# Performance work log

Measured on AMD Instinct MI355X. Metric: run time of the kernel, lower is better.

The kernel has to match this reference:

```python
import jax, jax.numpy as jnp
import numpy as np


def setup_inputs() -> dict:
    key = jax.random.key(0)
    k1, k2, k3, k4 = jax.random.split(key, 4)
    B, N, Fin, Fout, K = 8, 256, 64, 64, 3
    H = jax.random.normal(k1, (B, N, N, Fin), dtype=jnp.float32)
    # static Chebyshev polynomial stacks T_0..T_{K-1} for origin / dest Laplacians
    cheb_L1 = jax.random.normal(k2, (K, N, N), dtype=jnp.float32) * 0.1
    cheb_L2 = jax.random.normal(k3, (K, N, N), dtype=jnp.float32) * 0.1
    # xavier_uniform over last two dims (fan_in=Fin, fan_out=Fout)
    limit = float(np.sqrt(6.0 / (Fin + Fout)))
    weights = jax.random.uniform(k4, (K, K, Fin, Fout), dtype=jnp.float32,
                                 minval=-limit, maxval=limit)
    bias = jnp.zeros((Fout,), dtype=jnp.float32)
    return {"H": H, "cheb_L1": cheb_L1, "cheb_L2": cheb_L2,
            "weights": weights, "bias": bias}


def reference(H, cheb_L1, cheb_L2, weights, bias):
    # H' = relu( sum_{i,j} T_i(L1) @_1 H @_2 T_j(L2) @_3 W_ij + b )
    # Step 1: left graph shift for all i at once: (K,B,N,N,F)
    H_x1 = jnp.einsum('kuv,bvwf->kbuwf', cheb_L1, H)
    # Step 2+3 fused: right shift by T_j, project by W_ij, accumulate over i,j
    out = jnp.einsum('kbuwf,lwz,klfo->buzo', H_x1, cheb_L2, weights)
    return jax.nn.relu(out + bias)
```

## Files before the change

kernel.cpp:

```cpp
#include <hip/hip_runtime.h>

typedef __attribute__((ext_vector_type(8))) short s16x8;
typedef __attribute__((ext_vector_type(4))) float f32x4;

#define MFMA16 __builtin_amdgcn_mfma_f32_16x16x32_bf16

__device__ __forceinline__ short f2bf(float x) {
  union { float f; unsigned u; } c; c.f = x;
  unsigned r = (c.u + 0x7fffu + ((c.u >> 16) & 1u)) >> 16;
  return (short)r;
}

__device__ __forceinline__ void gld16(const void* g, void* l) {
  __builtin_amdgcn_global_load_lds(
      (const __attribute__((address_space(1))) unsigned*)g,
      (__attribute__((address_space(3))) unsigned*)l, 16, 0, 0);
}


__global__ __launch_bounds__(256) void k_cvt_l1(const float* __restrict__ L1,
                                                short* __restrict__ L1b) {
  int i = blockIdx.x * 256 + threadIdx.x;
  L1b[i] = f2bf(L1[i]);
}

__global__ __launch_bounds__(256) void k_build_l2cat(const float* __restrict__ L2,
                                                     short* __restrict__ L2cat) {
  __shared__ float t[32][33];
  const int l = blockIdx.z, w0 = blockIdx.x * 32, z0 = blockIdx.y * 32;
  const int tx = threadIdx.x, ty = threadIdx.y;
  const float* src = L2 + (size_t)l * 65536;
  for (int i = ty; i < 32; i += 8) t[i][tx] = src[(size_t)(w0 + i) * 256 + z0 + tx];
  __syncthreads();
  for (int i = ty; i < 32; i += 8)
    L2cat[(size_t)(z0 + i) * 768 + l * 256 + w0 + tx] = f2bf(t[tx][i]);
}

__global__ __launch_bounds__(256) void k_build_wt(const float* __restrict__ W,
                                                  short* __restrict__ WT) {
  for (int idx = threadIdx.x + blockIdx.x * 256; idx < 192 * 192; idx += 256 * gridDim.x) {
    int lo = idx / 192, kf = idx % 192;
    int l = lo >> 6, o = lo & 63, k = kf / 64, f = kf & 63;
    WT[idx] = f2bf(W[(((size_t)(k * 3 + l) * 64 + f) << 6) + o]);
  }
}

__global__ __launch_bounds__(256) void k_cvt_ht(const float* __restrict__ H,
                                                short* __restrict__ HbT, int b0) {
  __shared__ float t[32][33];
  const int bc = blockIdx.z;
  const int wf0 = blockIdx.x * 32, v0 = blockIdx.y * 32;
  const int tx = threadIdx.x, ty = threadIdx.y;
  const float* src = H + ((size_t)(b0 + bc) * 256 + v0) * 16384;
  for (int i = ty; i < 32; i += 8) t[i][tx] = src[(size_t)i * 16384 + wf0 + tx];
  __syncthreads();
  short* dst = HbT + ((size_t)bc * 16384 + wf0) * 256;
  for (int i = ty; i < 32; i += 8) dst[(size_t)i * 256 + v0 + tx] = f2bf(t[tx][i]);
}

__global__ __launch_bounds__(256) void k_s1(const short* __restrict__ L1b,
                                            const short* __restrict__ HbT,
                                            short* __restrict__ A2) {
  __shared__ __align__(16) short At[128 * 32];
  __shared__ __align__(16) short Bt[128 * 32];
  const int t = threadIdx.x, lane = t & 63, wid = t >> 6;
  const int n0 = blockIdx.x * 128;
  const int kk = blockIdx.y >> 1;
  const int u0 = (blockIdx.y & 1) * 128;
  const int bc = blockIdx.z;
  const short* Ag = L1b + (size_t)kk * 65536;
  const short* Bg = HbT + (size_t)bc * 16384 * 256;
  const int wm = wid >> 1, wn = wid & 1;
  const int srow = lane >> 2;
  const int selem = ((lane & 3) ^ ((lane >> 3) & 3)) * 8;
  const int koff = (((lane >> 4) ^ ((lane >> 1) & 3)) * 8);
  f32x4 acc[4][4] = {};
  for (int kt = 0; kt < 256; kt += 32) {
#pragma unroll
    for (int j = 0; j < 2; ++j) {
      const int rb = wid * 32 + j * 16;
      gld16(Ag + (size_t)(u0 + rb + srow) * 256 + kt + selem, (short*)At + (size_t)rb * 32);
      gld16(Bg + (size_t)(n0 + rb + srow) * 256 + kt + selem, (short*)Bt + (size_t)rb * 32);
    }
    __syncthreads();
    const int ar = lane & 15;
    s16x8 a[4], b[4];
#pragma unroll
    for (int i = 0; i < 4; ++i) a[i] = *(const s16x8*)&At[(wm * 64 + i * 16 + ar) * 32 + koff];
#pragma unroll
    for (int j = 0; j < 4; ++j) b[j] = *(const s16x8*)&Bt[(wn * 64 + j * 16 + ar) * 32 + koff];
#pragma unroll
    for (int i = 0; i < 4; ++i)
#pragma unroll
      for (int j = 0; j < 4; ++j) acc[i][j] = MFMA16(a[i], b[j], acc[i][j], 0, 0, 0);
    __syncthreads();
  }
  const int cr = lane >> 4, cc = lane & 15;
#pragma unroll
  for (int i = 0; i < 4; ++i)
#pragma unroll
    for (int j = 0; j < 4; ++j) {
      const int ncol = n0 + wn * 64 + j * 16 + cc;
      const int w = ncol >> 6, f = ncol & 63;
#pragma unroll
      for (int r = 0; r < 4; ++r) {
        const int u = u0 + wm * 64 + i * 16 + cr * 4 + r;
        A2[(((size_t)bc * 256 + u) * 256 + w) * 192 + kk * 64 + f] = f2bf(acc[i][j][r]);
      }
    }
}

__global__ __launch_bounds__(512) void k_s23(const short* __restrict__ A2,
                                             const short* __restrict__ WT,
                                             const short* __restrict__ L2cat,
                                             const float* __restrict__ bias,
                                             float* __restrict__ out, int b0) {
  __shared__ __align__(16) short P[64 * 768];
  __shared__ __align__(16) short At[256 * 64];
  __shared__ __align__(16) short Bs[192 * 64];
  const int t = threadIdx.x, lane = t & 63, wid = t >> 6;
  const int bul = blockIdx.x;
  const int ar = lane & 15, cc = lane & 15, cr = lane >> 4;
  const int selem = ((lane & 7) ^ ((lane >> 3) & 7)) * 8;
  const int ko0 = (((lane >> 4)) ^ (lane & 7)) * 8;
  const int ko1 = ((4 + (lane >> 4)) ^ (lane & 7)) * 8;
  const int srow8 = lane >> 3;

  f32x4 acc[3][2][4] = {};
  const short* A2g = A2 + (size_t)bul * 256 * 192;
  for (int kt = 0; kt < 192; kt += 64) {
#pragma unroll
    for (int is = 0; is < 4; ++is) {
      const int rb = wid * 32 + is * 8;
      gld16(A2g + (size_t)(rb + srow8) * 192 + kt + selem, (short*)At + (size_t)rb * 64);
    }
#pragma unroll
    for (int is = 0; is < 3; ++is) {
      const int rb = wid * 24 + is * 8;
      gld16(WT + (size_t)(rb + srow8) * 192 + kt + selem, (short*)Bs + (size_t)rb * 64);
    }
    __syncthreads();
    s16x8 a0[2], a1[2];
#pragma unroll
    for (int i = 0; i < 2; ++i) {
      a0[i] = *(const s16x8*)&At[(wid * 32 + i * 16 + ar) * 64 + ko0];
      a1[i] = *(const s16x8*)&At[(wid * 32 + i * 16 + ar) * 64 + ko1];
    }
#pragma unroll
    for (int l = 0; l < 3; ++l)
#pragma unroll
      for (int j = 0; j < 4; ++j) {
        s16x8 b0v = *(const s16x8*)&Bs[(l * 64 + j * 16 + ar) * 64 + ko0];
        s16x8 b1v = *(const s16x8*)&Bs[(l * 64 + j * 16 + ar) * 64 + ko1];
#pragma unroll
        for (int i = 0; i < 2; ++i) {
          acc[l][i][j] = MFMA16(a0[i], b0v, acc[l][i][j], 0, 0, 0);
          acc[l][i][j] = MFMA16(a1[i], b1v, acc[l][i][j], 0, 0, 0);
        }
      }
    __syncthreads();
  }
#pragma unroll
  for (int l = 0; l < 3; ++l)
#pragma unroll
    for (int i = 0; i < 2; ++i)
#pragma unroll
      for (int j = 0; j < 4; ++j)
#pragma unroll
        for (int rp = 0; rp < 2; ++rp) {
          const int r = rp * 2;
          const int w = wid * 32 + i * 16 + cr * 4 + r;
          const int o = j * 16 + cc;
          const int lw = l * 256 + w;
          const int addr = o * 768 + ((lw >> 3) ^ (o & 7)) * 8 + (lw & 7);
          unsigned lo16 = (unsigned short)f2bf(acc[l][i][j][r]);
          unsigned hi16 = (unsigned short)f2bf(acc[l][i][j][r + 1]);
          *(unsigned*)&P[addr] = lo16 | (hi16 << 16);
        }
  __syncthreads();

  f32x4 acc2[2][4] = {};
  for (int kt = 0; kt < 768; kt += 64) {
#pragma unroll
    for (int is = 0; is < 4; ++is) {
      const int rb = wid * 32 + is * 8;
      gld16(L2cat + (size_t)(rb + srow8) * 768 + kt + selem, (short*)At + (size_t)rb * 64);
    }
    __syncthreads();
    s16x8 a0[2], a1[2];
#pragma unroll
    for (int i = 0; i < 2; ++i) {
      a0[i] = *(const s16x8*)&At[(wid * 32 + i * 16 + ar) * 64 + ko0];
      a1[i] = *(const s16x8*)&At[(wid * 32 + i * 16 + ar) * 64 + ko1];
    }
#pragma unroll
    for (int j = 0; j < 4; ++j) {
      s16x8 b0v = *(const s16x8*)&P[(j * 16 + ar) * 768 + kt + ko0];
      s16x8 b1v = *(const s16x8*)&P[(j * 16 + ar) * 768 + kt + ko1];
#pragma unroll
      for (int i = 0; i < 2; ++i) {
        acc2[i][j] = MFMA16(a0[i], b0v, acc2[i][j], 0, 0, 0);
        acc2[i][j] = MFMA16(a1[i], b1v, acc2[i][j], 0, 0, 0);
      }
    }
    __syncthreads();
  }
  const int bu_g = b0 * 256 + bul;
  float* og = out + (size_t)bu_g * 256 * 64;
#pragma unroll
  for (int i = 0; i < 2; ++i)
#pragma unroll
    for (int j = 0; j < 4; ++j) {
      const float bv = bias[j * 16 + cc];
#pragma unroll
      for (int r = 0; r < 4; ++r) {
        const int z = wid * 32 + i * 16 + cr * 4 + r;
        og[(size_t)z * 64 + j * 16 + cc] = fmaxf(acc2[i][j][r] + bv, 0.f);
      }
    }
}

extern "C" void kernel_launch(void* const* d_in, const int* in_sizes, int n_in,
                              void* d_out, int out_size, void* d_ws, size_t ws_size,
                              hipStream_t stream) {
  const float* H    = (const float*)d_in[0];
  const float* L1   = (const float*)d_in[1];
  const float* L2   = (const float*)d_in[2];
  const float* W    = (const float*)d_in[3];
  const float* bias = (const float*)d_in[4];
  float* out = (float*)d_out;

  char* ws = (char*)d_ws;
  short* L1b   = (short*)ws;
  short* L2cat = (short*)(ws + (384 << 10));
  short* WT    = (short*)(ws + (768 << 10));
  char* data = ws + (4ull << 20);

  const size_t perb = 32ull << 20;
  size_t avail = (ws_size > (4ull << 20)) ? ws_size - (4ull << 20) : 0;
  int nb = 1;
  if (avail >= 8 * perb) nb = 8;
  else if (avail >= 4 * perb) nb = 4;
  else if (avail >= 2 * perb) nb = 2;

  short* HbT = (short*)data;
  short* A2  = (short*)(data + (size_t)nb * (8ull << 20));

  k_cvt_l1<<<768, 256, 0, stream>>>(L1, L1b);
  k_build_l2cat<<<dim3(8, 8, 3), dim3(32, 8), 0, stream>>>(L2, L2cat);
  k_build_wt<<<36, 256, 0, stream>>>(W, WT);

  for (int b0 = 0; b0 < 8; b0 += nb) {
    k_cvt_ht<<<dim3(512, 8, nb), dim3(32, 8), 0, stream>>>(H, HbT, b0);
    k_s1<<<dim3(128, 6, nb), 256, 0, stream>>>(L1b, HbT, A2);
    k_s23<<<nb * 256, 512, 0, stream>>>(A2, WT, L2cat, bias, out, b0);
  }
}
```

Before: 334.3 us.

## Double-buffer LDS loads in both GEMM kernels and split output channels across blocks

k_s1 gets double-buffered LDS tiles so the next K-slice global-to-LDS load overlaps the current MFMAs, with one barrier fewer per step. k_s23 is restructured: the grid doubles so each block handles half of the 64 output channels, and the full weight slice is preloaded into LDS. A2 and L2cat tiles are double-buffered with explicit vmcnt waits, and LDS is aliased to cut footprint so more blocks can be resident. The cost is redundant A2 and L2cat reads per half, and the intra-loop sync relies on vmcnt without workgroup barriers, which risks a race between waves sharing buffers.

```diff
diff --git a/kernel.cpp b/kernel.cpp
--- a/kernel.cpp
+++ b/kernel.cpp
@@ -4,6 +4,7 @@
 typedef __attribute__((ext_vector_type(4))) float f32x4;
 
 #define MFMA16 __builtin_amdgcn_mfma_f32_16x16x32_bf16
+#define WAIT_VM0() asm volatile("s_waitcnt vmcnt(0)" ::: "memory")
 
 __device__ __forceinline__ short f2bf(float x) {
   union { float f; unsigned u; } c; c.f = x;
@@ -58,11 +59,11 @@
   for (int i = ty; i < 32; i += 8) dst[(size_t)i * 256 + v0 + tx] = f2bf(t[tx][i]);
 }
 
-__global__ __launch_bounds__(256) void k_s1(const short* __restrict__ L1b,
-                                            const short* __restrict__ HbT,
-                                            short* __restrict__ A2) {
-  __shared__ __align__(16) short At[128 * 32];
-  __shared__ __align__(16) short Bt[128 * 32];
+__global__ __launch_bounds__(256, 4) void k_s1(const short* __restrict__ L1b,
+                                               const short* __restrict__ HbT,
+                                               short* __restrict__ A2) {
+  __shared__ __align__(16) short At[2][128 * 32];
+  __shared__ __align__(16) short Bt[2][128 * 32];
   const int t = threadIdx.x, lane = t & 63, wid = t >> 6;
   const int n0 = blockIdx.x * 128;
   const int kk = blockIdx.y >> 1;
@@ -73,22 +74,34 @@
   const int wm = wid >> 1, wn = wid & 1;
   const int srow = lane >> 2;
   const int selem = ((lane & 3) ^ ((lane >> 3) & 3)) * 8;
-  const int koff = (((lane >> 4) ^ ((lane >> 1) & 3)) * 8);
+  const int koff = ((lane >> 4) ^ ((lane >> 1) & 3)) * 8;
+  const int ar = lane & 15;
+#pragma unroll
+  for (int j = 0; j < 2; ++j) {
+    const int rb = wid * 32 + j * 16;
+    gld16(Ag + (size_t)(u0 + rb + srow) * 256 + selem, At[0] + rb * 32);
+    gld16(Bg + (size_t)(n0 + rb + srow) * 256 + selem, Bt[0] + rb * 32);
+  }
+  __syncthreads();
   f32x4 acc[4][4] = {};
-  for (int kt = 0; kt < 256; kt += 32) {
-#pragma unroll
-    for (int j = 0; j < 2; ++j) {
-      const int rb = wid * 32 + j * 16;
-      gld16(Ag + (size_t)(u0 + rb + srow) * 256 + kt + selem, (short*)At + (size_t)rb * 32);
-      gld16(Bg + (size_t)(n0 + rb + srow) * 256 + kt + selem, (short*)Bt + (size_t)rb * 32);
-    }
-    __syncthreads();
-    const int ar = lane & 15;
+#pragma unroll
+  for (int kt8 = 0; kt8 < 8; ++kt8) {
+    const int cur = kt8 & 1;
     s16x8 a[4], b[4];
 #pragma unroll
-    for (int i = 0; i < 4; ++i) a[i] = *(const s16x8*)&At[(wm * 64 + i * 16 + ar) * 32 + koff];
-#pragma unroll
-    for (int j = 0; j < 4; ++j) b[j] = *(const s16x8*)&Bt[(wn * 64 + j * 16 + ar) * 32 + koff];
+    for (int i = 0; i < 4; ++i)
+      a[i] = *(const s16x8*)&At[cur][(wm * 64 + i * 16 + ar) * 32 + koff];
+#pragma unroll
+    for (int j = 0; j < 4; ++j)
+      b[j] = *(const s16x8*)&Bt[cur][(wn * 64 + j * 16 + ar) * 32 + koff];
+    if (kt8 < 7) {
+#pragma unroll
+      for (int j = 0; j < 2; ++j) {
+        const int rb = wid * 32 + j * 16;
+        gld16(Ag + (size_t)(u0 + rb + srow) * 256 + (kt8 + 1) * 32 + selem, At[cur ^ 1] + rb * 32);
+        gld16(Bg + (size_t)(n0 + rb + srow) * 256 + (kt8 + 1) * 32 + selem, Bt[cur ^ 1] + rb * 32);
+      }
+    }
 #pragma unroll
     for (int i = 0; i < 4; ++i)
 #pragma unroll
@@ -110,62 +123,74 @@
     }
 }
 
-__global__ __launch_bounds__(512) void k_s23(const short* __restrict__ A2,
-                                             const short* __restrict__ WT,
-                                             const short* __restrict__ L2cat,
-                                             const float* __restrict__ bias,
-                                             float* __restrict__ out, int b0) {
-  __shared__ __align__(16) short P[64 * 768];
-  __shared__ __align__(16) short At[256 * 64];
-  __shared__ __align__(16) short Bs[192 * 64];
+__global__ __launch_bounds__(512, 4) void k_s23(const short* __restrict__ A2,
+                                                const short* __restrict__ WTg,
+                                                const short* __restrict__ L2cat,
+                                                const float* __restrict__ bias,
+                                                float* __restrict__ out, int b0) {
+  __shared__ __align__(16) char lds[81920];
+  short* P   = (short*)lds;
+  short* Ws  = (short*)lds;
+  short* AtS = (short*)(lds + 49152);
   const int t = threadIdx.x, lane = t & 63, wid = t >> 6;
-  const int bul = blockIdx.x;
-  const int ar = lane & 15, cc = lane & 15, cr = lane >> 4;
-  const int selem = ((lane & 7) ^ ((lane >> 3) & 7)) * 8;
-  const int ko0 = (((lane >> 4)) ^ (lane & 7)) * 8;
-  const int ko1 = ((4 + (lane >> 4)) ^ (lane & 7)) * 8;
-  const int srow8 = lane >> 3;
-
-  f32x4 acc[3][2][4] = {};
-  const short* A2g = A2 + (size_t)bul * 256 * 192;
-  for (int kt = 0; kt < 192; kt += 64) {
-#pragma unroll
-    for (int is = 0; is < 4; ++is) {
-      const int rb = wid * 32 + is * 8;
-      gld16(A2g + (size_t)(rb + srow8) * 192 + kt + selem, (short*)At + (size_t)rb * 64);
-    }
-#pragma unroll
-    for (int is = 0; is < 3; ++is) {
-      const int rb = wid * 24 + is * 8;
-      gld16(WT + (size_t)(rb + srow8) * 192 + kt + selem, (short*)Bs + (size_t)rb * 64);
-    }
-    __syncthreads();
-    s16x8 a0[2], a1[2];
-#pragma unroll
-    for (int i = 0; i < 2; ++i) {
-      a0[i] = *(const s16x8*)&At[(wid * 32 + i * 16 + ar) * 64 + ko0];
-      a1[i] = *(const s16x8*)&At[(wid * 32 + i * 16 + ar) * 64 + ko1];
-    }
+  const int bx = blockIdx.x;
+  const int bul = (bx & 7) | ((bx >> 4) << 3);
+  const int o0 = ((bx >> 3) & 1) * 32;
+  const int ar = lane & 15, cc = ar, cr = lane >> 4, sl = lane & 7;
+  const int srow = lane >> 2;
+  const int selem = ((lane & 3) ^ ((lane >> 3) & 3)) * 8;
+  const int koff = ((lane >> 4) ^ ((lane >> 1) & 3)) * 8;
+  const short* A2g = A2 + (size_t)bul * 49152;
+
+  for (int s = wid; s < 36; s += 8) {
+    const int t6 = s / 6, rb = (s % 6) * 16;
+    const int gr = (rb >> 5) * 64 + o0 + (rb & 31);
+    gld16(WTg + (size_t)(gr + srow) * 192 + t6 * 32 + selem, Ws + (t6 * 96 + rb) * 32);
+  }
+#pragma unroll
+  for (int is = 0; is < 2; ++is)
+    gld16(A2g + (size_t)(wid * 32 + is * 16 + srow) * 192 + selem,
+          AtS + (wid * 32 + is * 16) * 32);
+  __syncthreads();
+
+  f32x4 acc[3][2][2] = {};
+#pragma unroll
+  for (int kt6 = 0; kt6 < 6; ++kt6) {
+    const int cur = kt6 & 1;
+    WAIT_VM0();
+    s16x8 a[2];
+#pragma unroll
+    for (int i = 0; i < 2; ++i)
+      a[i] = *(const s16x8*)&AtS[(cur * 256 + wid * 32 + i * 16 + ar) * 32 + koff];
+    s16x8 b[3][2];
 #pragma unroll
     for (int l = 0; l < 3; ++l)
 #pragma unroll
-      for (int j = 0; j < 4; ++j) {
-        s16x8 b0v = *(const s16x8*)&Bs[(l * 64 + j * 16 + ar) * 64 + ko0];
-        s16x8 b1v = *(const s16x8*)&Bs[(l * 64 + j * 16 + ar) * 64 + ko1];
-#pragma unroll
-        for (int i = 0; i < 2; ++i) {
-          acc[l][i][j] = MFMA16(a0[i], b0v, acc[l][i][j], 0, 0, 0);
-          acc[l][i][j] = MFMA16(a1[i], b1v, acc[l][i][j], 0, 0, 0);
-        }
-      }
-    __syncthreads();
-  }
+      for (int j = 0; j < 2; ++j)
+        b[l][j] = *(const s16x8*)&Ws[(kt6 * 96 + l * 32 + j * 16 + ar) * 32 + koff];
+    if (kt6 < 5) {
+#pragma unroll
+      for (int is = 0; is < 2; ++is)
+        gld16(A2g + (size_t)(wid * 32 + is * 16 + srow) * 192 + (kt6 + 1) * 32 + selem,
+              AtS + ((cur ^ 1) * 256 + wid * 32 + is * 16) * 32);
+    }
+#pragma unroll
+    for (int l = 0; l < 3; ++l)
+#pragma unroll
+      for (int j = 0; j < 2; ++j)
+#pragma unroll
+        for (int i = 0; i < 2; ++i)
+          acc[l][j][i] = MFMA16(a[i], b[l][j], acc[l][j][i], 0, 0, 0);
+  }
+
+  __syncthreads();
+
 #pragma unroll
   for (int l = 0; l < 3; ++l)
 #pragma unroll
-    for (int i = 0; i < 2; ++i)
-#pragma unroll
-      for (int j = 0; j < 4; ++j)
+    for (int j = 0; j < 2; ++j)
+#pragma unroll
+      for (int i = 0; i < 2; ++i)
 #pragma unroll
         for (int rp = 0; rp < 2; ++rp) {
           const int r = rp * 2;
@@ -173,49 +198,53 @@
           const int o = j * 16 + cc;
           const int lw = l * 256 + w;
           const int addr = o * 768 + ((lw >> 3) ^ (o & 7)) * 8 + (lw & 7);
-          unsigned lo16 = (unsigned short)f2bf(acc[l][i][j][r]);
-          unsigned hi16 = (unsigned short)f2bf(acc[l][i][j][r + 1]);
+          unsigned lo16 = (unsigned short)f2bf(acc[l][j][i][r]);
+          unsigned hi16 = (unsigned short)f2bf(acc[l][j][i][r + 1]);
           *(unsigned*)&P[addr] = lo16 | (hi16 << 16);
         }
-  __syncthreads();
-
-  f32x4 acc2[2][4] = {};
-  for (int kt = 0; kt < 768; kt += 64) {
-#pragma unroll
-    for (int is = 0; is < 4; ++is) {
-      const int rb = wid * 32 + is * 8;
-      gld16(L2cat + (size_t)(rb + srow8) * 768 + kt + selem, (short*)At + (size_t)rb * 64);
-    }
-    __syncthreads();
-    s16x8 a0[2], a1[2];
-#pragma unroll
-    for (int i = 0; i < 2; ++i) {
-      a0[i] = *(const s16x8*)&At[(wid * 32 + i * 16 + ar) * 64 + ko0];
-      a1[i] = *(const s16x8*)&At[(wid * 32 + i * 16 + ar) * 64 + ko1];
-    }
-#pragma unroll
-    for (int j = 0; j < 4; ++j) {
-      s16x8 b0v = *(const s16x8*)&P[(j * 16 + ar) * 768 + kt + ko0];
-      s16x8 b1v = *(const s16x8*)&P[(j * 16 + ar) * 768 + kt + ko1];
-#pragma unroll
-      for (int i = 0; i < 2; ++i) {
-        acc2[i][j] = MFMA16(a0[i], b0v, acc2[i][j], 0, 0, 0);
-        acc2[i][j] = MFMA16(a1[i], b1v, acc2[i][j], 0, 0, 0);
-      }
-    }
-    __syncthreads();
-  }
-  const int bu_g = b0 * 256 + bul;
-  float* og = out + (size_t)bu_g * 256 * 64;
+#pragma unroll
+  for (int is = 0; is < 2; ++is)
+    gld16(L2cat + (size_t)(wid * 32 + is * 16 + srow) * 768 + selem,
+          AtS + (wid * 32 + is * 16) * 32);
+  __syncthreads();
+
+  f32x4 acc2[2][2] = {};
+#pragma unroll
+  for (int t2 = 0; t2 < 24; ++t2) {
+    const int cur = t2 & 1;
+    const int kt = t2 * 32;
+    WAIT_VM0();
+    s16x8 a[2], b[2];
+#pragma unroll
+    for (int i = 0; i < 2; ++i)
+      a[i] = *(const s16x8*)&AtS[(cur * 256 + wid * 32 + i * 16 + ar) * 32 + koff];
+#pragma unroll
+    for (int j = 0; j < 2; ++j) {
+      const int S = (kt >> 3) + (lane >> 4);
+      b[j] = *(const s16x8*)&P[(j * 16 + ar) * 768 + (S ^ sl) * 8];
+    }
+    if (t2 < 23) {
+#pragma unroll
+      for (int is = 0; is < 2; ++is)
+        gld16(L2cat + (size_t)(wid * 32 + is * 16 + srow) * 768 + (t2 + 1) * 32 + selem,
+              AtS + ((cur ^ 1) * 256 + wid * 32 + is * 16) * 32);
+    }
+#pragma unroll
+    for (int i = 0; i < 2; ++i)
+#pragma unroll
+      for (int j = 0; j < 2; ++j) acc2[i][j] = MFMA16(a[i], b[j], acc2[i][j], 0, 0, 0);
+  }
+
+  float* og = out + ((size_t)b0 * 256 + bul) * 16384;
 #pragma unroll
   for (int i = 0; i < 2; ++i)
 #pragma unroll
-    for (int j = 0; j < 4; ++j) {
-      const float bv = bias[j * 16 + cc];
+    for (int j = 0; j < 2; ++j) {
+      const float bv = bias[o0 + j * 16 + cc];
 #pragma unroll
       for (int r = 0; r < 4; ++r) {
         const int z = wid * 32 + i * 16 + cr * 4 + r;
-        og[(size_t)z * 64 + j * 16 + cc] = fmaxf(acc2[i][j][r] + bv, 0.f);
+        og[(size_t)z * 64 + o0 + j * 16 + cc] = fmaxf(acc2[i][j][r] + bv, 0.f);
       }
     }
 }
@@ -253,6 +282,6 @@
   for (int b0 = 0; b0 < 8; b0 += nb) {
     k_cvt_ht<<<dim3(512, 8, nb), dim3(32, 8), 0, stream>>>(H, HbT, b0);
     k_s1<<<dim3(128, 6, nb), 256, 0, stream>>>(L1b, HbT, A2);
-    k_s23<<<nb * 256, 512, 0, stream>>>(A2, WT, L2cat, bias, out, b0);
-  }
-}
+    k_s23<<<nb * 512, 512, 0, stream>>>(A2, WT, L2cat, bias, out, b0);
+  }
+}
```

New measurement: 352.1 us. +5.3%, slower.
